# Performance work log

Measured on AMD Instinct MI355X. Metric: run time of the kernel, lower is better.

## Reference

```python
import math
import jax, jax.numpy as jnp
import numpy as np

S, D = 4096, 2048
H, DH = 16, 128
ROPE_BASE = 10000.0


def _rotate_half(x):
    # x: [..., dh]; pairs (x1, x2) -> (-x2, x1), interleaved
    shp = x.shape
    x = x.reshape(*shp[:-1], shp[-1] // 2, 2)
    x1, x2 = x[..., 0], x[..., 1]
    return jnp.stack((-x2, x1), axis=-1).reshape(shp)


def _rope_cos_sin(seq_len, dh):
    inv_freq = 1.0 / (ROPE_BASE ** (jnp.arange(0, dh, 2, dtype=jnp.float32) / dh))
    t = jnp.arange(seq_len, dtype=jnp.float32)
    freqs = jnp.einsum('i,j->ij', t, inv_freq)  # [S, dh/2]
    cos = jnp.repeat(jnp.cos(freqs), 2, axis=-1)  # [S, dh]
    sin = jnp.repeat(jnp.sin(freqs), 2, axis=-1)
    return cos, sin


def setup_inputs() -> dict:
    key = jax.random.key(0)
    kx, kq, kk, kv, ko = jax.random.split(key, 5)
    scale_in = 1.0 / math.sqrt(D)
    scale_hd = 1.0 / math.sqrt(H * DH)
    return {
        'x': jax.random.normal(kx, (S, D), dtype=jnp.float32),
        'mask': jnp.tril(jnp.ones((S, S), dtype=bool)),  # causal
        'wq': jax.random.normal(kq, (H * DH, D), dtype=jnp.float32) * scale_in,
        'wk': jax.random.normal(kk, (H * DH, D), dtype=jnp.float32) * scale_in,
        'wv': jax.random.normal(kv, (H * DH, D), dtype=jnp.float32) * scale_in,
        'wo': jax.random.normal(ko, (D, H * DH), dtype=jnp.float32) * scale_hd,
    }


def reference(x, mask, wq, wk, wv, wo):
    s = x.shape[0]
    # QKV projections (Linear: y = W @ x per token) -> [h, S, dh]
    q = (x @ wq.T).reshape(s, H, DH).transpose(1, 0, 2)
    k = (x @ wk.T).reshape(s, H, DH).transpose(1, 0, 2)
    v = (x @ wv.T).reshape(s, H, DH).transpose(1, 0, 2)
    # RoPE
    cos, sin = _rope_cos_sin(s, DH)  # [S, dh] each
    q = q * cos[None] + _rotate_half(q) * sin[None]
    k = k * cos[None] + _rotate_half(k) * sin[None]
    # Attention
    sim = jnp.einsum('hid,hjd->hij', q, k) / math.sqrt(DH)  # [h, S, S]
    sim = jnp.where(mask[None], sim, -jnp.inf)
    attn = jax.nn.softmax(sim, axis=-1)
    out = jnp.einsum('hij,hjd->ihd', attn, v).reshape(s, H * DH)
    return out @ wo.T
```

## Files before the change

### kernel.cpp

```cpp
#include <hip/hip_runtime.h>
#include <stdint.h>

#define S_LEN 4096
#define D_MODEL 2048
#define NH 16
#define DH 128

typedef short s16x8 __attribute__((ext_vector_type(8)));
typedef short s16x2 __attribute__((ext_vector_type(2)));
typedef unsigned short u16;
typedef unsigned short u16x4 __attribute__((ext_vector_type(4)));
typedef float f32x4 __attribute__((ext_vector_type(4)));

__device__ __forceinline__ u16 f2bf(float f) {
  union { float f; uint32_t u; } v; v.f = f;
  uint32_t u = v.u;
  u += 0x7FFFu + ((u >> 16) & 1u);
  return (u16)(u >> 16);
}

__device__ __forceinline__ float bf2f(u16 b) {
  union { uint32_t u; float f; } v; v.u = ((uint32_t)b) << 16;
  return v.f;
}

__device__ __forceinline__ void async_copy16(const u16* g, u16* l) {
  __builtin_amdgcn_global_load_lds(
      (const __attribute__((address_space(1))) unsigned int*)g,
      (__attribute__((address_space(3))) unsigned int*)l, 16, 0, 0);
}

__global__ void cast_kernel(const float4* __restrict__ src, u16* __restrict__ dst, int n4) {
  int i = blockIdx.x * blockDim.x + threadIdx.x;
  if (i >= n4) return;
  float4 v = src[i];
  u16x4 o;
  o[0] = f2bf(v.x); o[1] = f2bf(v.y); o[2] = f2bf(v.z); o[3] = f2bf(v.w);
  *(u16x4*)(dst + (size_t)i * 4) = o;
}

__global__ void cast4_kernel(const float4* __restrict__ s0, const float4* __restrict__ s1,
                             const float4* __restrict__ s2, const float4* __restrict__ s3,
                             u16* __restrict__ d0, u16* __restrict__ d1,
                             u16* __restrict__ d2, u16* __restrict__ d3) {
  int b = blockIdx.x;
  int which = b >> 12;
  const float4* src = which == 0 ? s0 : which == 1 ? s1 : which == 2 ? s2 : s3;
  u16* dst = which == 0 ? d0 : which == 1 ? d1 : which == 2 ? d2 : d3;
  int i = (b & 4095) * blockDim.x + threadIdx.x;
  float4 v = src[i];
  u16x4 o;
  o[0] = f2bf(v.x); o[1] = f2bf(v.y); o[2] = f2bf(v.z); o[3] = f2bf(v.w);
  *(u16x4*)(dst + (size_t)i * 4) = o;
}

__global__ void rope_table(float* __restrict__ ctab, float* __restrict__ stab) {
  int idx = blockIdx.x * blockDim.x + threadIdx.x;
  int t = idx >> 6, p = idx & 63;
  float invf = powf(10000.0f, -(float)p / 64.0f);
  float th = (float)t * invf;
  ctab[idx] = cosf(th);
  stab[idx] = sinf(th);
}

__global__ __launch_bounds__(256) void gemm_qkv(
    const u16* __restrict__ A,
    const u16* __restrict__ wqb, const u16* __restrict__ wkb, const u16* __restrict__ wvb,
    u16* __restrict__ qh, u16* __restrict__ kh, u16* __restrict__ vh,
    const float* __restrict__ ctab, const float* __restrict__ stab)
{
  __shared__ __align__(16) u16 la[128 * 64];
  __shared__ __align__(16) u16 lb[128 * 64];
  const int tid = threadIdx.x;
  const int w = tid >> 6, lane = tid & 63, quad = lane >> 4, l16 = lane & 15;
  const int wm = (w & 1) << 6, wn = (w >> 1) << 6;
  const int m0 = blockIdx.x << 7;
  const int n0g = blockIdx.y << 7;
  const int which = n0g >> 11;
  const int n0 = n0g & 2047;
  const u16* B = which == 0 ? wqb : which == 1 ? wkb : wvb;
  u16* outp = which == 0 ? qh : which == 1 ? kh : vh;
  const int K = D_MODEL;

  f32x4 zero = {0.f, 0.f, 0.f, 0.f};
  f32x4 acc[4][4];
#pragma unroll
  for (int i = 0; i < 4; ++i)
#pragma unroll
    for (int j = 0; j < 4; ++j) acc[i][j] = zero;

  for (int k0 = 0; k0 < K; k0 += 64) {
    __syncthreads();
#pragma unroll
    for (int rnd = 0; rnd < 4; ++rnd) {
      int c = rnd * 256 + w * 64 + lane;
      int r = c >> 3, cc = c & 7;
      int gcol = ((cc ^ (r & 7)) << 3);
      int base = (rnd * 256 + w * 64) << 3;
      async_copy16(A + (size_t)(m0 + r) * K + k0 + gcol, la + base);
      async_copy16(B + (size_t)(n0 + r) * K + k0 + gcol, lb + base);
    }
    __syncthreads();
#pragma unroll
    for (int ks = 0; ks < 2; ++ks) {
      s16x8 af[4], bfr[4];
#pragma unroll
      for (int t = 0; t < 4; ++t) {
        int rowa = wm + (t << 4) + l16;
        af[t] = *(const s16x8*)(la + (rowa << 6) + ((((ks << 2) + quad) ^ (rowa & 7)) << 3));
        int rowb = wn + (t << 4) + l16;
        bfr[t] = *(const s16x8*)(lb + (rowb << 6) + ((((ks << 2) + quad) ^ (rowb & 7)) << 3));
      }
#pragma unroll
      for (int mt = 0; mt < 4; ++mt)
#pragma unroll
        for (int nt = 0; nt < 4; ++nt)
          acc[mt][nt] = __builtin_amdgcn_mfma_f32_16x16x32_bf16(af[mt], bfr[nt], acc[mt][nt], 0, 0, 0);
    }
  }

#pragma unroll
  for (int mt = 0; mt < 4; ++mt) {
    int rowg = m0 + wm + (mt << 4) + (quad << 2);
#pragma unroll
    for (int nt = 0; nt < 4; ++nt) {
      int cl = n0 + wn + (nt << 4) + l16;
      int hh = cl >> 7, dd = cl & 127;
      int p = dd >> 1;
      f32x4 v = acc[mt][nt];
#pragma unroll
      for (int r = 0; r < 4; ++r) {
        float val = v[r];
        if (which < 2) {
          float partner = __shfl_xor(val, 1);
          float c = ctab[(size_t)(rowg + r) * 64 + p];
          float s = stab[(size_t)(rowg + r) * 64 + p];
          val = (dd & 1) ? fmaf(val, c, partner * s) : fmaf(val, c, -partner * s);
        }
        outp[((size_t)hh * S_LEN + (rowg + r)) * DH + dd] = f2bf(val);
      }
    }
  }
}

__global__ __launch_bounds__(256) void gemm_bf16(
    const u16* __restrict__ A, const u16* __restrict__ B,
    float* __restrict__ outF, int M, int N, int K)
{
  __shared__ __align__(16) u16 la[128 * 64];
  __shared__ __align__(16) u16 lb[128 * 64];
  const int tid = threadIdx.x;
  const int w = tid >> 6, lane = tid & 63, quad = lane >> 4, l16 = lane & 15;
  const int wm = (w & 1) << 6, wn = (w >> 1) << 6;
  const int m0 = blockIdx.x << 7, n0 = blockIdx.y << 7;

  f32x4 zero = {0.f, 0.f, 0.f, 0.f};
  f32x4 acc[4][4];
#pragma unroll
  for (int i = 0; i < 4; ++i)
#pragma unroll
    for (int j = 0; j < 4; ++j) acc[i][j] = zero;

  for (int k0 = 0; k0 < K; k0 += 64) {
    __syncthreads();
#pragma unroll
    for (int rnd = 0; rnd < 4; ++rnd) {
      int c = rnd * 256 + w * 64 + lane;
      int r = c >> 3, cc = c & 7;
      int gcol = ((cc ^ (r & 7)) << 3);
      int base = (rnd * 256 + w * 64) << 3;
      async_copy16(A + (size_t)(m0 + r) * K + k0 + gcol, la + base);
      async_copy16(B + (size_t)(n0 + r) * K + k0 + gcol, lb + base);
    }
    __syncthreads();
#pragma unroll
    for (int ks = 0; ks < 2; ++ks) {
      s16x8 af[4], bfr[4];
#pragma unroll
      for (int t = 0; t < 4; ++t) {
        int rowa = wm + (t << 4) + l16;
        af[t] = *(const s16x8*)(la + (rowa << 6) + ((((ks << 2) + quad) ^ (rowa & 7)) << 3));
        int rowb = wn + (t << 4) + l16;
        bfr[t] = *(const s16x8*)(lb + (rowb << 6) + ((((ks << 2) + quad) ^ (rowb & 7)) << 3));
      }
#pragma unroll
      for (int mt = 0; mt < 4; ++mt)
#pragma unroll
        for (int nt = 0; nt < 4; ++nt)
          acc[mt][nt] = __builtin_amdgcn_mfma_f32_16x16x32_bf16(af[mt], bfr[nt], acc[mt][nt], 0, 0, 0);
    }
  }

#pragma unroll
  for (int mt = 0; mt < 4; ++mt) {
    int rowg = m0 + wm + (mt << 4) + (quad << 2);
#pragma unroll
    for (int nt = 0; nt < 4; ++nt) {
      int col = n0 + wn + (nt << 4) + l16;
      f32x4 v = acc[mt][nt];
#pragma unroll
      for (int r = 0; r < 4; ++r) outF[(size_t)(rowg + r) * N + col] = v[r];
    }
  }
}

__global__ __launch_bounds__(512) void attn_kernel(
    const u16* __restrict__ Q, const u16* __restrict__ Kb,
    const u16* __restrict__ V,
    u16* __restrict__ U0, u16* __restrict__ U1, float* __restrict__ lbuf)
{
  __shared__ __align__(16) u16 lk[2][64 * 128];
  __shared__ __align__(16) u16 lvt[2][128 * 64];
  __shared__ __align__(16) u16 lp[8 * 1024];

  const int tid = threadIdx.x;
  const int w = tid >> 6, lane = tid & 63, quad = lane >> 4, l16 = lane & 15;
  const int h = blockIdx.y;
  const int bx = blockIdx.x;

  const u16* Qh = Q + (size_t)h * S_LEN * DH;
  const u16* Kh = Kb + (size_t)h * S_LEN * DH;
  const u16* Vh = V + (size_t)h * S_LEN * DH;

  const float scale = 0.08838834764831845f;
  const s16x8 vones = {0x3F80, 0x3F80, 0x3F80, 0x3F80, 0x3F80, 0x3F80, 0x3F80, 0x3F80};
  f32x4 zero = {0.f, 0.f, 0.f, 0.f};
  u16* lpw = lp + (w << 10);

  for (int seg = 0; seg < 2; ++seg) {
    const int qt = seg ? bx : (31 - bx);
    const int jlo = seg ? (qt + 1) : 0;
    const int jhi = seg ? (2 * qt + 2) : (qt + 1);
    const int i0 = qt << 7;
    const int iw = i0 + (w << 4);

    s16x8 qf[4];
#pragma unroll
    for (int ks = 0; ks < 4; ++ks)
      qf[ks] = *(const s16x8*)(Qh + (size_t)(iw + l16) * DH + ks * 32 + quad * 8);

    f32x4 accO[8];
#pragma unroll
    for (int dt = 0; dt < 8; ++dt) accO[dt] = zero;
    f32x4 accL = zero;

    {
      const int j0 = jlo << 6;
      int u = tid & 31, c8 = tid >> 5, r0 = u << 1;
      s16x8 v0 = *(const s16x8*)(Vh + (size_t)(j0 + r0) * DH + (c8 << 3));
      s16x8 v1 = *(const s16x8*)(Vh + (size_t)(j0 + r0 + 1) * DH + (c8 << 3));
#pragma unroll
      for (int rnd = 0; rnd < 2; ++rnd) {
        int c = rnd * 512 + tid;
        int r = c >> 4, cc = c & 15;
        int gcol = ((cc ^ (r & 15)) << 3);
        async_copy16(Kh + (size_t)(j0 + r) * DH + gcol, lk[0] + ((rnd * 512 + w * 64) << 3));
      }
      int cc = r0 >> 3;
#pragma unroll
      for (int e = 0; e < 8; ++e) {
        int d = (c8 << 3) + e;
        int off = (d << 6) + ((cc ^ (d & 7)) << 3) + (r0 & 7);
        s16x2 pr = {v0[e], v1[e]};
        *(s16x2*)(lvt[0] + off) = pr;
      }
    }
    __syncthreads();

    int cur = 0;
    for (int jt = jlo; jt < jhi; ++jt) {
      const int j0 = jt << 6;
      const bool has_next = (jt + 1) < jhi;

      s16x8 nv0, nv1;
      if (has_next) {
        const int nj0 = (jt + 1) << 6;
        int u = tid & 31, c8 = tid >> 5, r0 = u << 1;
        nv0 = *(const s16x8*)(Vh + (size_t)(nj0 + r0) * DH + (c8 << 3));
        nv1 = *(const s16x8*)(Vh + (size_t)(nj0 + r0 + 1) * DH + (c8 << 3));
#pragma unroll
        for (int rnd = 0; rnd < 2; ++rnd) {
          int c = rnd * 512 + tid;
          int r = c >> 4, cc = c & 15;
          int gcol = ((cc ^ (r & 15)) << 3);
          async_copy16(Kh + (size_t)(nj0 + r) * DH + gcol,
                       lk[cur ^ 1] + ((rnd * 512 + w * 64) << 3));
        }
      }

      const u16* lkc = lk[cur];
      f32x4 sa[4];
#pragma unroll
      for (int nt = 0; nt < 4; ++nt) sa[nt] = zero;
      __builtin_amdgcn_s_setprio(1);
#pragma unroll
      for (int ks = 0; ks < 4; ++ks) {
#pragma unroll
        for (int nt = 0; nt < 4; ++nt) {
          int row = (nt << 4) + l16;
          s16x8 kf = *(const s16x8*)(lkc + (row << 7) + ((((ks << 2) + quad) ^ (row & 15)) << 3));
          sa[nt] = __builtin_amdgcn_mfma_f32_16x16x32_bf16(qf[ks], kf, sa[nt], 0, 0, 0);
        }
      }
      __builtin_amdgcn_s_setprio(0);

      const bool maskt = (j0 + 63 > iw);
#pragma unroll
      for (int nt = 0; nt < 4; ++nt) {
        int col = (nt << 4) + l16;
        int j = j0 + col;
        int ccp = col >> 3;
#pragma unroll
        for (int r = 0; r < 4; ++r) {
          float raw = sa[nt][r];
          if (maskt) {
            int i = iw + (quad << 2) + r;
            if (j > i) raw = -1.0e30f;
          }
          float p = __expf(fmaf(raw, scale, -8.0f));
          union { float f; uint32_t u; } pv; pv.f = p;
          int m = (quad << 2) + r;
          lpw[(m << 6) + ((ccp ^ (m & 7)) << 3) + (col & 7)] = (u16)(pv.u >> 16);
        }
      }
      asm volatile("s_waitcnt lgkmcnt(0)" ::: "memory");
      s16x8 pf[2];
#pragma unroll
      for (int kp = 0; kp < 2; ++kp)
        pf[kp] = *(const s16x8*)(lpw + (l16 << 6) + ((((kp << 2) + quad) ^ (l16 & 7)) << 3));

      if (has_next) {
        int u = tid & 31, c8 = tid >> 5, r0 = u << 1;
        int cc = r0 >> 3;
        u16* dst = lvt[cur ^ 1];
#pragma unroll
        for (int e = 0; e < 8; ++e) {
          int d = (c8 << 3) + e;
          int off = (d << 6) + ((cc ^ (d & 7)) << 3) + (r0 & 7);
          s16x2 pr = {nv0[e], nv1[e]};
          *(s16x2*)(dst + off) = pr;
        }
      }

      const u16* lvc = lvt[cur];
      __builtin_amdgcn_s_setprio(1);
      accL = __builtin_amdgcn_mfma_f32_16x16x32_bf16(pf[0], vones, accL, 0, 0, 0);
      accL = __builtin_amdgcn_mfma_f32_16x16x32_bf16(pf[1], vones, accL, 0, 0, 0);
#pragma unroll
      for (int dt = 0; dt < 8; ++dt) {
#pragma unroll
        for (int kp = 0; kp < 2; ++kp) {
          int row = (dt << 4) + l16;
          s16x8 vf = *(const s16x8*)(lvc + (row << 6) + ((((kp << 2) + quad) ^ (row & 7)) << 3));
          accO[dt] = __builtin_amdgcn_mfma_f32_16x16x32_bf16(pf[kp], vf, accO[dt], 0, 0, 0);
        }
      }
      __builtin_amdgcn_s_setprio(0);

      __syncthreads();
      cur ^= 1;
    }

    u16* Useg = seg ? U1 : U0;
    float* ls = lbuf + (size_t)seg * NH * S_LEN + (size_t)h * S_LEN;
#pragma unroll
    for (int r = 0; r < 4; ++r) {
      float lr = accL[r];
      float inv = lr > 0.f ? 1.0f / lr : 0.f;
      int srow = iw + (quad << 2) + r;
#pragma unroll
      for (int dt = 0; dt < 8; ++dt)
        Useg[((size_t)h * S_LEN + srow) * DH + (dt << 4) + l16] = f2bf(accO[dt][r] * inv);
      if (l16 == 0) ls[srow] = lr;
    }
  }
}

__global__ void combine_kernel(const u16* __restrict__ U0, const u16* __restrict__ U1,
                               const float* __restrict__ lbuf, u16* __restrict__ ob)
{
  int t = blockIdx.x * 256 + threadIdx.x;
  int d8 = t & 15;
  int h = (t >> 4) & 15;
  int s = t >> 8;
  float l0 = lbuf[(size_t)h * S_LEN + s];
  float l1 = lbuf[(size_t)(NH * S_LEN) + (size_t)h * S_LEN + s];
  float inv = 1.0f / (l0 + l1);
  float w0 = l0 * inv, w1 = l1 * inv;
  size_t base = ((size_t)h * S_LEN + s) * DH + d8 * 8;
  s16x8 u0 = *(const s16x8*)(U0 + base);
  s16x8 u1 = *(const s16x8*)(U1 + base);
  u16 o[8];
#pragma unroll
  for (int e = 0; e < 8; ++e)
    o[e] = f2bf(w0 * bf2f((u16)u0[e]) + w1 * bf2f((u16)u1[e]));
  *(s16x8*)(ob + ((size_t)s * D_MODEL + h * DH + d8 * 8)) = *(s16x8*)o;
}

extern "C" void kernel_launch(void* const* d_in, const int* in_sizes, int n_in,
                              void* d_out, int out_size, void* d_ws, size_t ws_size,
                              hipStream_t stream) {
  const float* x  = (const float*)d_in[0];
  const float* wq = (const float*)d_in[2];
  const float* wk = (const float*)d_in[3];
  const float* wv = (const float*)d_in[4];
  const float* wo = (const float*)d_in[5];
  float* out = (float*)d_out;

  char* ws = (char*)d_ws;
  u16* xb  = (u16*)(ws);
  u16* wqb = (u16*)(ws + (16ull << 20));
  u16* wkb = (u16*)(ws + (24ull << 20));
  u16* wvb = (u16*)(ws + (32ull << 20));
  u16* wob = (u16*)(ws + (40ull << 20));
  u16* qh  = (u16*)(ws + (48ull << 20));
  u16* kh  = (u16*)(ws + (64ull << 20));
  u16* vh  = (u16*)(ws + (80ull << 20));
  float* ctab = (float*)(ws + (96ull << 20));
  float* stab = (float*)(ws + (97ull << 20));
  u16* U0 = (u16*)(ws);
  u16* U1 = (u16*)(ws + (16ull << 20));
  float* lbuf = (float*)(ws + (32ull << 20));
  u16* ob = qh;

  const int nx4 = S_LEN * D_MODEL / 4;
  cast_kernel<<<nx4 / 256, 256, 0, stream>>>((const float4*)x, xb, nx4);
  cast4_kernel<<<4 * 4096, 256, 0, stream>>>(
      (const float4*)wq, (const float4*)wk, (const float4*)wv, (const float4*)wo,
      wqb, wkb, wvb, wob);
  rope_table<<<(S_LEN * 64) / 256, 256, 0, stream>>>(ctab, stab);

  gemm_qkv<<<dim3(S_LEN / 128, 3 * D_MODEL / 128), 256, 0, stream>>>(
      xb, wqb, wkb, wvb, qh, kh, vh, ctab, stab);

  attn_kernel<<<dim3(32, NH), 512, 0, stream>>>(qh, kh, vh, U0, U1, lbuf);
  combine_kernel<<<S_LEN * NH * 16 / 256, 256, 0, stream>>>(U0, U1, lbuf, ob);

  gemm_bf16<<<dim3(S_LEN / 128, D_MODEL / 128), 256, 0, stream>>>(
      ob, wob, out, S_LEN, D_MODEL, D_MODEL);
}
```

Measured before the change: 510.7 us.

## Replace projection GEMMs with 256x256 tiled, double-buffered, 8-wave pipelined MFMA core

Result: no change. 510.8 us (+0.0%).

```diff
diff --git a/kernel.cpp b/kernel.cpp
--- a/kernel.cpp
+++ b/kernel.cpp
@@ -63,71 +63,151 @@
   stab[idx] = sinf(th);
 }
 
-__global__ __launch_bounds__(256) void gemm_qkv(
+#define G256_BAR() __builtin_amdgcn_s_barrier()
+#define G256_LGK0() do { asm volatile("s_waitcnt lgkmcnt(0)" ::: "memory"); \
+                         __builtin_amdgcn_sched_barrier(0); } while (0)
+#define G256_VMC4() asm volatile("s_waitcnt vmcnt(4)" ::: "memory")
+
+__device__ __forceinline__ void stage128(const u16* __restrict__ src, u16* dst,
+                                         int rr, int gc, int ldk) {
+  const u16* s = src + (size_t)rr * ldk + gc;
+  u16* d = dst + (threadIdx.x << 3);
+  async_copy16(s, d);
+  async_copy16(s + (size_t)64 * ldk, d + 4096);
+}
+
+__device__ __forceinline__ void mma256_core(
+    const u16* __restrict__ Ab,
+    const u16* __restrict__ Bb,
+    const int K, u16* lds, f32x4 (&acc)[8][4])
+{
+  const int tid = threadIdx.x;
+  const int lane = tid & 63, quad = lane >> 4, l16 = lane & 15;
+  const int w = tid >> 6, wr = w >> 2, wc = w & 3;
+  const int rr = tid >> 3;
+  const int gc = ((tid & 7) ^ (rr & 7)) << 3;
+
+  u16* const A0b = lds;
+  u16* const B0b = lds + 16384;
+  u16* const A1b = lds + 32768;
+  u16* const B1b = lds + 49152;
+
+  const int NT = K >> 6;
+
+  auto sA = [&](int t, int hh, u16* buf) {
+    int tc = t < NT ? t : NT - 1;
+    stage128(Ab + (size_t)(hh << 7) * K + ((size_t)tc << 6), buf + (hh << 13), rr, gc, K);
+  };
+  auto sB = [&](int t, int hh, u16* buf) {
+    int tc = t < NT ? t : NT - 1;
+    stage128(Bb + (size_t)(hh << 7) * K + ((size_t)tc << 6), buf + (hh << 13), rr, gc, K);
+  };
+
+  s16x8 a[4][2], b[4][2];
+  auto rA = [&](const u16* buf, int mh) {
+#pragma unroll
+    for (int mt = 0; mt < 4; ++mt) {
+      int ra = (wr << 7) + (mh << 6) + (mt << 4) + l16;
+#pragma unroll
+      for (int ks = 0; ks < 2; ++ks)
+        a[mt][ks] = *(const s16x8*)(buf + (ra << 6) + ((((ks << 2) + quad) ^ (ra & 7)) << 3));
+    }
+  };
+  auto rB = [&](const u16* buf, int nh) {
+#pragma unroll
+    for (int nt = 0; nt < 2; ++nt) {
+      int rb = (wc << 6) + (((nh << 1) + nt) << 4) + l16;
+#pragma unroll
+      for (int ks = 0; ks < 2; ++ks)
+        b[(nh << 1) + nt][ks] =
+            *(const s16x8*)(buf + (rb << 6) + ((((ks << 2) + quad) ^ (rb & 7)) << 3));
+    }
+  };
+  auto mmaq = [&](int mh, int nh) {
+    __builtin_amdgcn_s_setprio(1);
+#pragma unroll
+    for (int mt = 0; mt < 4; ++mt)
+#pragma unroll
+      for (int nt = 0; nt < 2; ++nt) {
+#pragma unroll
+        for (int ks = 0; ks < 2; ++ks)
+          acc[(mh << 2) + mt][(nh << 1) + nt] = __builtin_amdgcn_mfma_f32_16x16x32_bf16(
+              a[mt][ks], b[(nh << 1) + nt][ks], acc[(mh << 2) + mt][(nh << 1) + nt], 0, 0, 0);
+      }
+    __builtin_amdgcn_s_setprio(0);
+  };
+
+  sB(0, 0, B0b); sB(0, 1, B0b); sA(0, 0, A0b); sA(0, 1, A0b);
+  sB(1, 0, B1b); sB(1, 1, B1b);
+  G256_VMC4();
+  G256_BAR();
+
+  const int NI = K >> 7;
+#pragma unroll 1
+  for (int i = 0; i < NI; ++i) {
+    const int t1 = 2 * i + 1, t2 = 2 * i + 2, t3 = 2 * i + 3;
+    sA(t1, 0, A1b);
+    rA(A0b, 0); rB(B0b, 0);
+    G256_BAR(); G256_LGK0(); mmaq(0, 0); G256_BAR();
+    sA(t1, 1, A1b);
+    rB(B0b, 1);
+    G256_BAR(); G256_LGK0(); mmaq(0, 1); G256_BAR();
+    sB(t2, 0, B0b);
+    rA(A0b, 1);
+    G256_BAR(); G256_LGK0(); mmaq(1, 0); G256_BAR();
+    sB(t2, 1, B0b);
+    G256_VMC4();
+    G256_BAR(); mmaq(1, 1); G256_BAR();
+    sA(t2, 0, A0b);
+    rA(A1b, 0); rB(B1b, 0);
+    G256_BAR(); G256_LGK0(); mmaq(0, 0); G256_BAR();
+    sA(t2, 1, A0b);
+    rB(B1b, 1);
+    G256_BAR(); G256_LGK0(); mmaq(0, 1); G256_BAR();
+    sB(t3, 0, B1b);
+    rA(A1b, 1);
+    G256_BAR(); G256_LGK0(); mmaq(1, 0); G256_BAR();
+    sB(t3, 1, B1b);
+    G256_VMC4();
+    G256_BAR(); mmaq(1, 1); G256_BAR();
+  }
+}
+
+__global__ __launch_bounds__(512) void gemm256_qkv(
     const u16* __restrict__ A,
     const u16* __restrict__ wqb, const u16* __restrict__ wkb, const u16* __restrict__ wvb,
     u16* __restrict__ qh, u16* __restrict__ kh, u16* __restrict__ vh,
     const float* __restrict__ ctab, const float* __restrict__ stab)
 {
-  __shared__ __align__(16) u16 la[128 * 64];
-  __shared__ __align__(16) u16 lb[128 * 64];
+  __shared__ __align__(16) u16 lds[65536];
   const int tid = threadIdx.x;
-  const int w = tid >> 6, lane = tid & 63, quad = lane >> 4, l16 = lane & 15;
-  const int wm = (w & 1) << 6, wn = (w >> 1) << 6;
-  const int m0 = blockIdx.x << 7;
-  const int n0g = blockIdx.y << 7;
-  const int which = n0g >> 11;
-  const int n0 = n0g & 2047;
+  const int lane = tid & 63, quad = lane >> 4, l16 = lane & 15;
+  const int w = tid >> 6, wr = w >> 2, wc = w & 3;
+  const int m0 = blockIdx.x << 8;
+  const int by = blockIdx.y;
+  const int which = by >> 3;
+  const int n0 = (by & 7) << 8;
   const u16* B = which == 0 ? wqb : which == 1 ? wkb : wvb;
   u16* outp = which == 0 ? qh : which == 1 ? kh : vh;
-  const int K = D_MODEL;
-
+
+  f32x4 acc[8][4];
   f32x4 zero = {0.f, 0.f, 0.f, 0.f};
-  f32x4 acc[4][4];
-#pragma unroll
-  for (int i = 0; i < 4; ++i)
+#pragma unroll
+  for (int i = 0; i < 8; ++i)
 #pragma unroll
     for (int j = 0; j < 4; ++j) acc[i][j] = zero;
 
-  for (int k0 = 0; k0 < K; k0 += 64) {
-    __syncthreads();
-#pragma unroll
-    for (int rnd = 0; rnd < 4; ++rnd) {
-      int c = rnd * 256 + w * 64 + lane;
-      int r = c >> 3, cc = c & 7;
-      int gcol = ((cc ^ (r & 7)) << 3);
-      int base = (rnd * 256 + w * 64) << 3;
-      async_copy16(A + (size_t)(m0 + r) * K + k0 + gcol, la + base);
-      async_copy16(B + (size_t)(n0 + r) * K + k0 + gcol, lb + base);
-    }
-    __syncthreads();
-#pragma unroll
-    for (int ks = 0; ks < 2; ++ks) {
-      s16x8 af[4], bfr[4];
-#pragma unroll
-      for (int t = 0; t < 4; ++t) {
-        int rowa = wm + (t << 4) + l16;
-        af[t] = *(const s16x8*)(la + (rowa << 6) + ((((ks << 2) + quad) ^ (rowa & 7)) << 3));
-        int rowb = wn + (t << 4) + l16;
-        bfr[t] = *(const s16x8*)(lb + (rowb << 6) + ((((ks << 2) + quad) ^ (rowb & 7)) << 3));
-      }
-#pragma unroll
-      for (int mt = 0; mt < 4; ++mt)
-#pragma unroll
-        for (int nt = 0; nt < 4; ++nt)
-          acc[mt][nt] = __builtin_amdgcn_mfma_f32_16x16x32_bf16(af[mt], bfr[nt], acc[mt][nt], 0, 0, 0);
-    }
-  }
-
-#pragma unroll
-  for (int mt = 0; mt < 4; ++mt) {
-    int rowg = m0 + wm + (mt << 4) + (quad << 2);
-#pragma unroll
-    for (int nt = 0; nt < 4; ++nt) {
-      int cl = n0 + wn + (nt << 4) + l16;
+  mma256_core(A + (size_t)m0 * D_MODEL, B + (size_t)n0 * D_MODEL, D_MODEL, lds, acc);
+
+#pragma unroll
+  for (int Mt = 0; Mt < 8; ++Mt) {
+    int rowg = m0 + (wr << 7) + (Mt << 4) + (quad << 2);
+#pragma unroll
+    for (int Nt = 0; Nt < 4; ++Nt) {
+      int cl = n0 + (wc << 6) + (Nt << 4) + l16;
       int hh = cl >> 7, dd = cl & 127;
       int p = dd >> 1;
-      f32x4 v = acc[mt][nt];
+      f32x4 v = acc[Mt][Nt];
 #pragma unroll
       for (int r = 0; r < 4; ++r) {
         float val = v[r];
@@ -143,63 +223,33 @@
   }
 }
 
-__global__ __launch_bounds__(256) void gemm_bf16(
-    const u16* __restrict__ A, const u16* __restrict__ B,
-    float* __restrict__ outF, int M, int N, int K)
+__global__ __launch_bounds__(512) void gemm256_out(
+    const u16* __restrict__ A, const u16* __restrict__ B, float* __restrict__ outF)
 {
-  __shared__ __align__(16) u16 la[128 * 64];
-  __shared__ __align__(16) u16 lb[128 * 64];
+  __shared__ __align__(16) u16 lds[65536];
   const int tid = threadIdx.x;
-  const int w = tid >> 6, lane = tid & 63, quad = lane >> 4, l16 = lane & 15;
-  const int wm = (w & 1) << 6, wn = (w >> 1) << 6;
-  const int m0 = blockIdx.x << 7, n0 = blockIdx.y << 7;
-
+  const int lane = tid & 63, quad = lane >> 4, l16 = lane & 15;
+  const int w = tid >> 6, wr = w >> 2, wc = w & 3;
+  const int m0 = blockIdx.x << 8, n0 = blockIdx.y << 8;
+
+  f32x4 acc[8][4];
   f32x4 zero = {0.f, 0.f, 0.f, 0.f};
-  f32x4 acc[4][4];
-#pragma unroll
-  for (int i = 0; i < 4; ++i)
+#pragma unroll
+  for (int i = 0; i < 8; ++i)
 #pragma unroll
     for (int j = 0; j < 4; ++j) acc[i][j] = zero;
 
-  for (int k0 = 0; k0 < K; k0 += 64) {
-    __syncthreads();
-#pragma unroll
-    for (int rnd = 0; rnd < 4; ++rnd) {
-      int c = rnd * 256 + w * 64 + lane;
-      int r = c >> 3, cc = c & 7;
-      int gcol = ((cc ^ (r & 7)) << 3);
-      int base = (rnd * 256 + w * 64) << 3;
-      async_copy16(A + (size_t)(m0 + r) * K + k0 + gcol, la + base);
-      async_copy16(B + (size_t)(n0 + r) * K + k0 + gcol, lb + base);
-    }
-    __syncthreads();
-#pragma unroll
-    for (int ks = 0; ks < 2; ++ks) {
-      s16x8 af[4], bfr[4];
-#pragma unroll
-      for (int t = 0; t < 4; ++t) {
-        int rowa = wm + (t << 4) + l16;
-        af[t] = *(const s16x8*)(la + (rowa << 6) + ((((ks << 2) + quad) ^ (rowa & 7)) << 3));
-        int rowb = wn + (t << 4) + l16;
-        bfr[t] = *(const s16x8*)(lb + (rowb << 6) + ((((ks << 2) + quad) ^ (rowb & 7)) << 3));
-      }
-#pragma unroll
-      for (int mt = 0; mt < 4; ++mt)
-#pragma unroll
-        for (int nt = 0; nt < 4; ++nt)
-          acc[mt][nt] = __builtin_amdgcn_mfma_f32_16x16x32_bf16(af[mt], bfr[nt], acc[mt][nt], 0, 0, 0);
-    }
-  }
-
-#pragma unroll
-  for (int mt = 0; mt < 4; ++mt) {
-    int rowg = m0 + wm + (mt << 4) + (quad << 2);
-#pragma unroll
-    for (int nt = 0; nt < 4; ++nt) {
-      int col = n0 + wn + (nt << 4) + l16;
-      f32x4 v = acc[mt][nt];
-#pragma unroll
-      for (int r = 0; r < 4; ++r) outF[(size_t)(rowg + r) * N + col] = v[r];
+  mma256_core(A + (size_t)m0 * D_MODEL, B + (size_t)n0 * D_MODEL, D_MODEL, lds, acc);
+
+#pragma unroll
+  for (int Mt = 0; Mt < 8; ++Mt) {
+    int rowg = m0 + (wr << 7) + (Mt << 4) + (quad << 2);
+#pragma unroll
+    for (int Nt = 0; Nt < 4; ++Nt) {
+      int col = n0 + (wc << 6) + (Nt << 4) + l16;
+      f32x4 v = acc[Mt][Nt];
+#pragma unroll
+      for (int r = 0; r < 4; ++r) outF[(size_t)(rowg + r) * D_MODEL + col] = v[r];
     }
   }
 }
@@ -430,12 +480,12 @@
       wqb, wkb, wvb, wob);
   rope_table<<<(S_LEN * 64) / 256, 256, 0, stream>>>(ctab, stab);
 
-  gemm_qkv<<<dim3(S_LEN / 128, 3 * D_MODEL / 128), 256, 0, stream>>>(
+  gemm256_qkv<<<dim3(S_LEN / 256, 3 * D_MODEL / 256), 512, 0, stream>>>(
       xb, wqb, wkb, wvb, qh, kh, vh, ctab, stab);
 
   attn_kernel<<<dim3(32, NH), 512, 0, stream>>>(qh, kh, vh, U0, U1, lbuf);
   combine_kernel<<<S_LEN * NH * 16 / 256, 256, 0, stream>>>(U0, U1, lbuf, ob);
 
-  gemm_bf16<<<dim3(S_LEN / 128, D_MODEL / 128), 256, 0, stream>>>(
-      ob, wob, out, S_LEN, D_MODEL, D_MODEL);
-}
+  gemm256_out<<<dim3(S_LEN / 256, D_MODEL / 256), 512, 0, stream>>>(
+      ob, wob, out);
+}
```
